# Optimization experiments

Measured on AMD Instinct MI355X. Metric: run time of the kernel, lower is better.

The kernel has to match this reference:

```python
import jax, jax.numpy as jnp
import numpy as np

T = 0.07          # cfg.CAP.TEMP
K = 50            # cfg.CAP.HARD_NEG_K
LOSS_WEIGHT = 0.5 # cfg.CAP.LOSS_WEIGHT
C_CAM = 8         # number of cameras
P = 2048          # pseudo-ID classes per camera bank


def setup_inputs() -> dict:
    key = jax.random.key(0)
    k1, k2, k3, k4 = jax.random.split(key, 4)
    B, D = 256, 2048
    inputs = jax.random.normal(k1, (B, D), jnp.float32)
    labels = jax.random.randint(k2, (B,), 0, P)
    cams = jax.random.randint(k3, (B,), 0, C_CAM)
    tempV = jax.random.normal(k4, (C_CAM * P, D), jnp.float32)
    tempV = tempV / jnp.linalg.norm(tempV, axis=1, keepdims=True)  # memory rows are L2-normalized
    return {"inputs": inputs, "labels": labels, "cams": cams, "tempV": tempV}


def _seg_mean_sum(vals, cams):
    # original loops over unique cams: loss += mean(vals within cam); empty cams contribute 0
    sums = jax.ops.segment_sum(vals, cams, num_segments=C_CAM)
    cnts = jax.ops.segment_sum(jnp.ones_like(vals), cams, num_segments=C_CAM)
    return jnp.sum(jnp.where(cnts > 0, sums / jnp.maximum(cnts, 1.0), 0.0))


def reference(inputs, labels, cams, tempV):
    B = inputs.shape[0]
    # cfg.CAP.NORM_FEAT
    x = inputs / jnp.linalg.norm(inputs, axis=1, keepdims=True)

    # one fused matmul against the concatenated memory; per-camera banks are contiguous P-slices
    all_logits = x @ tempV.T                      # [B, C_CAM*P]
    logits3 = all_logits.reshape(B, C_CAM, P)

    # ---- intra-camera loss: logits against the sample's own camera bank ----
    percam = jnp.take_along_axis(logits3, cams[:, None, None], axis=1)[:, 0, :] / T  # [B, P]
    lse_i = jax.scipy.special.logsumexp(percam, axis=1)
    ce = lse_i - jnp.take_along_axis(percam, labels[:, None], axis=1)[:, 0]
    loss_intra = _seg_mean_sum(ce, cams)

    # ---- inter-camera loss with hard-negative mining ----
    rows = jnp.arange(B)[:, None]
    # each ID has one centroid in every camera bank: positions label + P*cam
    ori_ind = labels[:, None] + P * jnp.arange(C_CAM)[None, :]        # [B, C_CAM]
    sims = all_logits.at[rows, ori_ind].set(-10000.0)                 # mask positives
    _, sel_ind = jax.lax.top_k(sims, K)                               # hard negatives (== sort[-K:])
    ori_logits = jnp.take_along_axis(all_logits, ori_ind, axis=1) / T  # [B, C_CAM]
    sel_logits = jnp.take_along_axis(all_logits, sel_ind, axis=1) / T  # [B, K]
    cat = jnp.concatenate([ori_logits, sel_logits], axis=1)            # [B, C_CAM+K]
    lse_c = jax.scipy.special.logsumexp(cat, axis=1)
    # target = 1/len(ori) on positives, 0 on negatives -> lse - mean(positive logits)
    loss_k = lse_c - jnp.mean(ori_logits, axis=1)
    loss_inter = LOSS_WEIGHT * _seg_mean_sum(loss_k, cams)

    return (loss_intra, loss_inter)
```

## Files before the change

kernel.cpp:

```cpp
#include <hip/hip_runtime.h>
#include <hip/hip_bf16.h>

#define BATCH 256
#define DIM   2048
#define NMEM  16384
#define PCLS  2048
#define CCAM  8
#define KSEL  50
#define T_INV 14.285714285714285714f
#define NB2   2048

typedef __bf16 bf16x8 __attribute__((ext_vector_type(8)));
typedef float  f32x4  __attribute__((ext_vector_type(4)));

static __device__ __forceinline__ unsigned int f2bf(float f) {
  unsigned int u = __float_as_uint(f);
  return (u + 0x7FFFu + ((u >> 16) & 1u)) >> 16;
}
static __device__ __forceinline__ unsigned int pk2(float lo, float hi) {
  return f2bf(lo) | (f2bf(hi) << 16);
}
static __device__ __forceinline__ int binw(float x, float lo, float scale) {
  int b = (int)((x - lo) * scale);
  return b > (NB2 - 1) ? (NB2 - 1) : b;
}

static __device__ __forceinline__ size_t pa_idx(int r, int c) {
  return (size_t)(r >> 4) * (size_t)(64 * 8 * (DIM / 32))
       + (size_t)(c >> 5) * 512
       + (size_t)(((r & 15) | (((c >> 3) & 3) << 4))) * 8
       + (size_t)(c & 7);
}

__global__ __launch_bounds__(256) void norm_cast_kernel(
    const float* __restrict__ in, unsigned short* __restrict__ xpk) {
  __shared__ float red[256];
  const int b = blockIdx.x, t = threadIdx.x;
  const float4* row = (const float4*)(in + (size_t)b * DIM);
  float4 a0 = row[t];
  float4 a1 = row[t + 256];
  float ss = a0.x*a0.x + a0.y*a0.y + a0.z*a0.z + a0.w*a0.w
           + a1.x*a1.x + a1.y*a1.y + a1.z*a1.z + a1.w*a1.w;
  red[t] = ss; __syncthreads();
  for (int s = 128; s > 0; s >>= 1) { if (t < s) red[t] += red[t + s]; __syncthreads(); }
  const float rn = rsqrtf(red[0]);
  ushort4 o0, o1;
  o0.x = (unsigned short)f2bf(a0.x*rn); o0.y = (unsigned short)f2bf(a0.y*rn);
  o0.z = (unsigned short)f2bf(a0.z*rn); o0.w = (unsigned short)f2bf(a0.w*rn);
  o1.x = (unsigned short)f2bf(a1.x*rn); o1.y = (unsigned short)f2bf(a1.y*rn);
  o1.z = (unsigned short)f2bf(a1.z*rn); o1.w = (unsigned short)f2bf(a1.w*rn);
  *(ushort4*)&xpk[pa_idx(b, 4 * t)]         = o0;
  *(ushort4*)&xpk[pa_idx(b, 4 * (t + 256))] = o1;
}

#define BMH 128
#define BNW 64
#define BKC 64
#define NCH (DIM / BKC)

__global__ __launch_bounds__(256, 2) void gemm_kernel(
    const unsigned short* __restrict__ Xpk,
    const float* __restrict__ V,
    float* __restrict__ C) {
  __shared__ __align__(16) unsigned short Bf[2][8][512];
  const int t    = threadIdx.x;
  const int lane = t & 63;
  const int wid  = t >> 6;
  const int n0 = blockIdx.x * BNW;
  const int m0 = blockIdx.y * BMH;

  const int vr = t >> 2;
  const int vq = t & 3;
  const float* Vp = V + (size_t)(n0 + vr) * DIM + vq * 16;
  const int wf = (vr >> 4) * 2 + (vq >> 1);
  const int wl = 32 * (vq & 1) + (vr & 15);

  const unsigned short* Apk = Xpk + (size_t)((m0 >> 4) + wid * 2) * 32768
                                  + (size_t)lane * 8;

  f32x4 acc[2][4];
#pragma unroll
  for (int i = 0; i < 2; i++)
#pragma unroll
    for (int j = 0; j < 4; j++) acc[i][j] = (f32x4){0.f, 0.f, 0.f, 0.f};

  bf16x8 aE[4], aO[4];
  float4 vE[4], vO[4];

#define LOADA(SET, ch)                                                        \
  {                                                                           \
    const int ck_ = (ch);                                                     \
    _Pragma("unroll")                                                         \
    for (int i = 0; i < 2; ++i)                                               \
      _Pragma("unroll")                                                       \
      for (int s = 0; s < 2; ++s)                                             \
        SET[i * 2 + s] = *(const bf16x8*)(Apk + (size_t)i * 32768             \
                                              + (size_t)(ck_ * 2 + s) * 512); \
  }
#define LOADV(VS, ch)                                                         \
  {                                                                           \
    const int ck_ = (ch);                                                     \
    _Pragma("unroll")                                                         \
    for (int g = 0; g < 4; ++g)                                               \
      VS[g] = *(const float4*)(Vp + ck_ * BKC + g * 4);                       \
  }
#define WRITEB(buf, VS)                                                       \
  {                                                                           \
    uint4 u0_, u1_;                                                           \
    u0_.x = pk2(VS[0].x, VS[0].y); u0_.y = pk2(VS[0].z, VS[0].w);             \
    u0_.z = pk2(VS[1].x, VS[1].y); u0_.w = pk2(VS[1].z, VS[1].w);             \
    u1_.x = pk2(VS[2].x, VS[2].y); u1_.y = pk2(VS[2].z, VS[2].w);             \
    u1_.z = pk2(VS[3].x, VS[3].y); u1_.w = pk2(VS[3].z, VS[3].w);             \
    *(uint4*)&Bf[buf][wf][(size_t)wl * 8]        = u0_;                       \
    *(uint4*)&Bf[buf][wf][(size_t)(wl + 16) * 8] = u1_;                       \
  }
#define COMPUTE(buf, ASET)                                                    \
  {                                                                           \
    _Pragma("unroll")                                                         \
    for (int s = 0; s < 2; ++s) {                                             \
      bf16x8 bF_[4];                                                          \
      _Pragma("unroll")                                                       \
      for (int j = 0; j < 4; ++j)                                             \
        bF_[j] = *(const bf16x8*)&Bf[buf][j * 2 + s][(size_t)lane * 8];       \
      _Pragma("unroll")                                                       \
      for (int i = 0; i < 2; ++i)                                             \
        _Pragma("unroll")                                                     \
        for (int j = 0; j < 4; ++j)                                           \
          acc[i][j] = __builtin_amdgcn_mfma_f32_16x16x32_bf16(                \
              ASET[i * 2 + s], bF_[j], acc[i][j], 0, 0, 0);                   \
    }                                                                         \
  }

  LOADA(aE, 0); LOADV(vE, 0);
  WRITEB(0, vE);
  LOADA(aO, 1); LOADV(vO, 1);
  __syncthreads();

#pragma unroll 1
  for (int it = 0; it < NCH / 2; ++it) {
    const int ch = 2 * it;
    LOADV(vE, min(ch + 2, NCH - 1));
    COMPUTE(0, aE);
    WRITEB(1, vO);
    LOADA(aE, min(ch + 2, NCH - 1));
    __syncthreads();
    LOADV(vO, min(ch + 3, NCH - 1));
    COMPUTE(1, aO);
    WRITEB(0, vE);
    LOADA(aO, min(ch + 3, NCH - 1));
    __syncthreads();
  }

  const int cr = (lane >> 4) * 4;
  const int cc = lane & 15;
#pragma unroll
  for (int i = 0; i < 2; i++)
#pragma unroll
    for (int j = 0; j < 4; j++)
#pragma unroll
      for (int r = 0; r < 4; r++)
        C[(size_t)(m0 + wid * 32 + i * 16 + cr + r) * NMEM + (n0 + j * 16 + cc)] =
            acc[i][j][r];
#undef LOADA
#undef LOADV
#undef WRITEB
#undef COMPUTE
}

__global__ __launch_bounds__(1024) void row_loss_kernel(
    const float* __restrict__ logits,
    const int* __restrict__ labels, const int* __restrict__ cams,
    float* __restrict__ ce_out, float* __restrict__ lossk_out) {
  __shared__ float ovs[CCAM];
  __shared__ float wredA[16], wredB[16];
  __shared__ int   hist[NB2];
  __shared__ int   pint[256];
  __shared__ float bl[512];
  __shared__ int   bcount;
  __shared__ int   bstar_s, cabove_s, totwin_s;
  __shared__ float vmax_s;

  const int b = blockIdx.x, t = threadIdx.x;
  const int lane = t & 63, wid = t >> 6;
  const int cam = cams[b], label = labels[b];
  const float* row = logits + (size_t)b * NMEM;

  if (t < CCAM) ovs[t] = row[t * PCLS + label];

  float4 rr[4];
#pragma unroll
  for (int i = 0; i < 4; i++) rr[i] = *(const float4*)(row + (size_t)(t + 1024 * i) * 4);

  float vmax = -1e30f, Si = 0.f;
#pragma unroll
  for (int i = 0; i < 4; i++) {
    const int base = (t + 1024 * i) * 4;
    const float xs[4] = {rr[i].x, rr[i].y, rr[i].z, rr[i].w};
#pragma unroll
    for (int e = 0; e < 4; e++) {
      const int n = base + e;
      const float x = xs[e];
      if ((n >> 11) == cam) Si += __expf(x * T_INV);
      if ((n & (PCLS - 1)) != label) vmax = fmaxf(vmax, x);
    }
  }
#pragma unroll
  for (int off = 32; off > 0; off >>= 1) {
    vmax = fmaxf(vmax, __shfl_down(vmax, off));
    Si  += __shfl_down(Si, off);
  }
  if (lane == 0) { wredA[wid] = vmax; wredB[wid] = Si; }
  __syncthreads();
  if (t == 0) {
    float m = -1e30f, s = 0.f;
    for (int i = 0; i < 16; i++) { m = fmaxf(m, wredA[i]); s += wredB[i]; }
    vmax_s = m;
    ce_out[b] = logf(s) - ovs[cam] * T_INV;
    bcount = 0;
  }
  __syncthreads();

  float W = 0.0625f;
  float lo = 0.f, scale = 0.f;
  for (int att = 0; att < 6; ++att) {
    __syncthreads();
    for (int i = t; i < NB2; i += 1024) hist[i] = 0;
    __syncthreads();
    lo = vmax_s - W; scale = (float)NB2 / W;
#pragma unroll
    for (int i = 0; i < 4; i++) {
      const int base = (t + 1024 * i) * 4;
      const float xs[4] = {rr[i].x, rr[i].y, rr[i].z, rr[i].w};
#pragma unroll
      for (int e = 0; e < 4; e++) {
        const int n = base + e;
        const float x = xs[e];
        if (((n & (PCLS - 1)) != label) && x >= lo)
          atomicAdd(&hist[binw(x, lo, scale)], 1);
      }
    }
    __syncthreads();
    if (t < 256) {
      int ps = 0;
#pragma unroll
      for (int i = 0; i < 8; i++) ps += hist[t * 8 + i];
      pint[t] = ps;
    }
    __syncthreads();
    if (t == 0) {
      int tot = 0;
      for (int i = 0; i < 256; i++) tot += pint[i];
      totwin_s = tot;
      if (tot >= KSEL) {
        int cum = 0, bstar = 0, cab = 0;
        for (int tc = 255; tc >= 0; tc--) {
          if (cum + pint[tc] >= KSEL) {
            for (int bi = tc * 8 + 7; bi >= tc * 8; bi--) {
              int h = hist[bi];
              if (cum + h >= KSEL) { bstar = bi; cab = cum; break; }
              cum += h;
            }
            break;
          }
          cum += pint[tc];
        }
        bstar_s = bstar; cabove_s = cab;
      }
    }
    __syncthreads();
    if (totwin_s >= KSEL) break;
    W *= 8.f;
  }
  const int bstar = bstar_s;

  float S2 = 0.f;
#pragma unroll
  for (int i = 0; i < 4; i++) {
    const int base = (t + 1024 * i) * 4;
    const float xs[4] = {rr[i].x, rr[i].y, rr[i].z, rr[i].w};
#pragma unroll
    for (int e = 0; e < 4; e++) {
      const int n = base + e;
      const float x = xs[e];
      if (((n & (PCLS - 1)) != label) && x >= lo) {
        const int bin = binw(x, lo, scale);
        if (bin > bstar) S2 += __expf(x * T_INV);
        else if (bin == bstar) {
          int p = atomicAdd(&bcount, 1);
          if (p < 512) bl[p] = x;
        }
      }
    }
  }
#pragma unroll
  for (int off = 32; off > 0; off >>= 1) S2 += __shfl_down(S2, off);
  if (lane == 0) wredB[wid] = S2;
  __syncthreads();

  if (t == 0) {
    float S2tot = 0.f;
    for (int i = 0; i < 16; i++) S2tot += wredB[i];
    const int need = KSEL - cabove_s;
    const int bc = min(bcount, 512);
    for (int r = 0; r < need; r++) {
      float mx = -1e30f; int mi = 0;
      for (int i = 0; i < bc; i++) if (bl[i] > mx) { mx = bl[i]; mi = i; }
      S2tot += __expf(mx * T_INV);
      bl[mi] = -1e30f;
    }
    float sumo = 0.f;
#pragma unroll
    for (int c = 0; c < CCAM; c++) { S2tot += __expf(ovs[c] * T_INV); sumo += ovs[c]; }
    lossk_out[b] = logf(S2tot) - (sumo * T_INV) * (1.0f / CCAM);
  }
}

__global__ __launch_bounds__(256) void finalize_kernel(
    const float* __restrict__ ce, const float* __restrict__ lossk,
    const int* __restrict__ cams, float* __restrict__ out) {
  __shared__ float ce_s[BATCH], lk_s[BATCH];
  __shared__ int   cam_s[BATCH];
  __shared__ float si[CCAM], sk[CCAM], cnt[CCAM];
  const int t = threadIdx.x;
  ce_s[t]  = ce[t];
  lk_s[t]  = lossk[t];
  cam_s[t] = cams[t];
  __syncthreads();
  if (t < CCAM) {
    float a = 0.f, b = 0.f; int n = 0;
    for (int i = 0; i < BATCH; i++) {
      if (cam_s[i] == t) { a += ce_s[i]; b += lk_s[i]; n++; }
    }
    si[t] = a; sk[t] = b; cnt[t] = (float)n;
  }
  __syncthreads();
  if (t == 0) {
    float li = 0.f, lk = 0.f;
    for (int c = 0; c < CCAM; c++) {
      if (cnt[c] > 0.f) { li += si[c] / cnt[c]; lk += sk[c] / cnt[c]; }
    }
    out[0] = li;
    out[1] = 0.5f * lk;
  }
}

extern "C" void kernel_launch(void* const* d_in, const int* in_sizes, int n_in,
                              void* d_out, int out_size, void* d_ws, size_t ws_size,
                              hipStream_t stream) {
  const float* inputs = (const float*)d_in[0];
  const int*   labels = (const int*)d_in[1];
  const int*   cams   = (const int*)d_in[2];
  const float* tempV  = (const float*)d_in[3];
  float* out = (float*)d_out;

  char* ws = (char*)d_ws;
  unsigned short* xpk = (unsigned short*)ws;
  float* logits       = (float*)(ws + (1u << 20));
  float* ce           = (float*)(ws + (1u << 20) + (16u << 20));
  float* lossk        = (float*)(ws + (1u << 20) + (16u << 20) + 1024);

  norm_cast_kernel<<<BATCH, 256, 0, stream>>>(inputs, xpk);
  gemm_kernel<<<dim3(NMEM / BNW, BATCH / BMH), 256, 0, stream>>>(xpk, tempV, logits);
  row_loss_kernel<<<BATCH, 1024, 0, stream>>>(logits, labels, cams, ce, lossk);
  finalize_kernel<<<1, 256, 0, stream>>>(ce, lossk, cams, out);
}
```

Measured before the change: 256.8 us.

## Retile GEMM waves to 2x2 grid with manual waitcnt-controlled prefetch pipeline

The four waves in the GEMM block are rearranged from a 4x1 layout (each wave covering 32 rows by all 64 columns) into a 2x2 layout (64 rows by 32 columns). Each wave now reads half as many B fragments from LDS while loading twice as many A fragments from global memory. The V loads are re-laid-out with a strided column pattern and written to LDS as 8-byte stores. __syncthreads is replaced by explicit s_waitcnt vmcnt/lgkmcnt plus s_barrier and sched_barrier so that global prefetch stays in flight while the MFMAs run. This raises register pressure and depends on a hand-counted vmcnt value being correct.

```diff
diff --git a/kernel.cpp b/kernel.cpp
--- a/kernel.cpp
+++ b/kernel.cpp
@@ -66,103 +66,116 @@
   const int t    = threadIdx.x;
   const int lane = t & 63;
   const int wid  = t >> 6;
+  const int widM = wid >> 1, widN = wid & 1;
   const int n0 = blockIdx.x * BNW;
   const int m0 = blockIdx.y * BMH;
 
-  const int vr = t >> 2;
-  const int vq = t & 3;
-  const float* Vp = V + (size_t)(n0 + vr) * DIM + vq * 16;
-  const int wf = (vr >> 4) * 2 + (vq >> 1);
-  const int wl = 32 * (vq & 1) + (vr & 15);
-
-  const unsigned short* Apk = Xpk + (size_t)((m0 >> 4) + wid * 2) * 32768
+  const int vr  = t >> 2;
+  const int vc4 = (t & 3) * 4;
+  const float* Vp = V + (size_t)(n0 + vr) * DIM + vc4;
+  const int wfr = vr & 15, wjn = vr >> 4;
+
+  const unsigned short* Apk = Xpk + (size_t)((m0 >> 4) + widM * 4) * 32768
                                   + (size_t)lane * 8;
 
-  f32x4 acc[2][4];
-#pragma unroll
-  for (int i = 0; i < 2; i++)
-#pragma unroll
-    for (int j = 0; j < 4; j++) acc[i][j] = (f32x4){0.f, 0.f, 0.f, 0.f};
-
-  bf16x8 aE[4], aO[4];
-  float4 vE[4], vO[4];
-
-#define LOADA(SET, ch)                                                        \
-  {                                                                           \
-    const int ck_ = (ch);                                                     \
-    _Pragma("unroll")                                                         \
-    for (int i = 0; i < 2; ++i)                                               \
-      _Pragma("unroll")                                                       \
-      for (int s = 0; s < 2; ++s)                                             \
-        SET[i * 2 + s] = *(const bf16x8*)(Apk + (size_t)i * 32768             \
-                                              + (size_t)(ck_ * 2 + s) * 512); \
-  }
+  f32x4 acc[4][2];
+#pragma unroll
+  for (int i = 0; i < 4; i++)
+#pragma unroll
+    for (int j = 0; j < 2; j++) acc[i][j] = (f32x4){0.f, 0.f, 0.f, 0.f};
+
+  bf16x8 aA[8], aB[8];
+  float4 vA[4], vB[4];
+
 #define LOADV(VS, ch)                                                         \
   {                                                                           \
     const int ck_ = (ch);                                                     \
     _Pragma("unroll")                                                         \
     for (int g = 0; g < 4; ++g)                                               \
-      VS[g] = *(const float4*)(Vp + ck_ * BKC + g * 4);                       \
+      VS[g] = *(const float4*)(Vp + ck_ * BKC + g * 16);                      \
+  }
+#define LOADA(AS, ch)                                                         \
+  {                                                                           \
+    const int ck_ = (ch);                                                     \
+    _Pragma("unroll")                                                         \
+    for (int i = 0; i < 4; ++i)                                               \
+      _Pragma("unroll")                                                       \
+      for (int s = 0; s < 2; ++s)                                             \
+        AS[i * 2 + s] = *(const bf16x8*)(Apk + (size_t)i * 32768              \
+                                             + (size_t)(ck_ * 2 + s) * 512);  \
   }
 #define WRITEB(buf, VS)                                                       \
   {                                                                           \
-    uint4 u0_, u1_;                                                           \
-    u0_.x = pk2(VS[0].x, VS[0].y); u0_.y = pk2(VS[0].z, VS[0].w);             \
-    u0_.z = pk2(VS[1].x, VS[1].y); u0_.w = pk2(VS[1].z, VS[1].w);             \
-    u1_.x = pk2(VS[2].x, VS[2].y); u1_.y = pk2(VS[2].z, VS[2].w);             \
-    u1_.z = pk2(VS[3].x, VS[3].y); u1_.w = pk2(VS[3].z, VS[3].w);             \
-    *(uint4*)&Bf[buf][wf][(size_t)wl * 8]        = u0_;                       \
-    *(uint4*)&Bf[buf][wf][(size_t)(wl + 16) * 8] = u1_;                       \
-  }
-#define COMPUTE(buf, ASET)                                                    \
+    _Pragma("unroll")                                                         \
+    for (int g = 0; g < 4; ++g) {                                             \
+      const int c_  = vc4 + g * 16;                                           \
+      const int f_  = wjn * 2 + (c_ >> 5);                                    \
+      const int sl_ = (((c_ & 31) >> 3) << 4) + wfr;                          \
+      uint2 p_; p_.x = pk2(VS[g].x, VS[g].y); p_.y = pk2(VS[g].z, VS[g].w);   \
+      *(uint2*)&Bf[buf][f_][sl_ * 8 + (c_ & 7)] = p_;                         \
+    }                                                                         \
+  }
+#define COMPUTE(buf, AS)                                                      \
   {                                                                           \
-    _Pragma("unroll")                                                         \
-    for (int s = 0; s < 2; ++s) {                                             \
-      bf16x8 bF_[4];                                                          \
+    bf16x8 bF_[2][2];                                                         \
+    _Pragma("unroll")                                                         \
+    for (int j = 0; j < 2; ++j)                                               \
       _Pragma("unroll")                                                       \
-      for (int j = 0; j < 4; ++j)                                             \
-        bF_[j] = *(const bf16x8*)&Bf[buf][j * 2 + s][(size_t)lane * 8];       \
+      for (int s = 0; s < 2; ++s)                                             \
+        bF_[j][s] = *(const bf16x8*)&Bf[buf][(widN * 2 + j) * 2 + s]          \
+                                       [(size_t)lane * 8];                    \
+    asm volatile("s_waitcnt vmcnt(12) lgkmcnt(0)" ::: "memory");              \
+    __builtin_amdgcn_sched_barrier(0);                                        \
+    _Pragma("unroll")                                                         \
+    for (int s = 0; s < 2; ++s)                                               \
       _Pragma("unroll")                                                       \
-      for (int i = 0; i < 2; ++i)                                             \
+      for (int i = 0; i < 4; ++i)                                             \
         _Pragma("unroll")                                                     \
-        for (int j = 0; j < 4; ++j)                                           \
+        for (int j = 0; j < 2; ++j)                                           \
           acc[i][j] = __builtin_amdgcn_mfma_f32_16x16x32_bf16(                \
-              ASET[i * 2 + s], bF_[j], acc[i][j], 0, 0, 0);                   \
-    }                                                                         \
-  }
-
-  LOADA(aE, 0); LOADV(vE, 0);
-  WRITEB(0, vE);
-  LOADA(aO, 1); LOADV(vO, 1);
-  __syncthreads();
+              AS[i * 2 + s], bF_[j][s], acc[i][j], 0, 0, 0);                  \
+  }
+
+  {
+    float4 v0[4];
+    LOADV(v0, 0);
+    asm volatile("s_waitcnt vmcnt(0)" ::: "memory");
+    WRITEB(0, v0);
+  }
+  LOADV(vA, 1);
+  LOADA(aA, 0);
+  asm volatile("s_waitcnt lgkmcnt(0)" ::: "memory");
+  __builtin_amdgcn_s_barrier();
 
 #pragma unroll 1
   for (int it = 0; it < NCH / 2; ++it) {
-    const int ch = 2 * it;
-    LOADV(vE, min(ch + 2, NCH - 1));
-    COMPUTE(0, aE);
-    WRITEB(1, vO);
-    LOADA(aE, min(ch + 2, NCH - 1));
-    __syncthreads();
-    LOADV(vO, min(ch + 3, NCH - 1));
-    COMPUTE(1, aO);
-    WRITEB(0, vE);
-    LOADA(aO, min(ch + 3, NCH - 1));
-    __syncthreads();
+    const int P0 = 2 * it;
+    LOADV(vB, min(P0 + 2, NCH - 1));
+    LOADA(aB, min(P0 + 1, NCH - 1));
+    COMPUTE(0, aA);
+    WRITEB(1, vA);
+    asm volatile("s_waitcnt lgkmcnt(0)" ::: "memory");
+    __builtin_amdgcn_s_barrier();
+    LOADV(vA, min(P0 + 3, NCH - 1));
+    LOADA(aA, min(P0 + 2, NCH - 1));
+    COMPUTE(1, aB);
+    WRITEB(0, vB);
+    asm volatile("s_waitcnt lgkmcnt(0)" ::: "memory");
+    __builtin_amdgcn_s_barrier();
   }
 
   const int cr = (lane >> 4) * 4;
   const int cc = lane & 15;
 #pragma unroll
-  for (int i = 0; i < 2; i++)
-#pragma unroll
-    for (int j = 0; j < 4; j++)
+  for (int i = 0; i < 4; i++)
+#pragma unroll
+    for (int j = 0; j < 2; j++)
 #pragma unroll
       for (int r = 0; r < 4; r++)
-        C[(size_t)(m0 + wid * 32 + i * 16 + cr + r) * NMEM + (n0 + j * 16 + cc)] =
-            acc[i][j][r];
+        C[(size_t)(m0 + widM * 64 + i * 16 + cr + r) * NMEM
+          + (n0 + widN * 32 + j * 16 + cc)] = acc[i][j][r];
+#undef LOADV
 #undef LOADA
-#undef LOADV
 #undef WRITEB
 #undef COMPUTE
 }
```

After: 257.3 us. About the same (+0.2%).
